# Performance work log

Hardware: AMD Instinct MI355X
Metric: run time of the kernel (lower is better)

The kernel has to match this reference:

```python
import jax, jax.numpy as jnp
import numpy as np

D_MODEL, Q, V, H = 1024, 64, 64, 16
B, K = 2, 2048


def setup_inputs() -> dict:
    key = jax.random.key(0)
    ks = jax.random.split(key, 8)
    s = 0.02
    return {
        "xi": jax.random.normal(ks[0], (B, K, D_MODEL), dtype=jnp.float32),
        # stacked per-head projection weights (equivalent to h separate nn.Linear)
        "Wq": jax.random.normal(ks[1], (H, D_MODEL, Q), dtype=jnp.float32) * s,
        "bq": jax.random.normal(ks[2], (H, Q), dtype=jnp.float32) * s,
        "Wk": jax.random.normal(ks[3], (H, D_MODEL, Q), dtype=jnp.float32) * s,
        "bk": jax.random.normal(ks[4], (H, Q), dtype=jnp.float32) * s,
        "Wv": jax.random.normal(ks[5], (H, D_MODEL, V), dtype=jnp.float32) * s,
        "bv": jax.random.normal(ks[6], (H, V), dtype=jnp.float32) * s,
        "Wo": jax.random.normal(ks[7], (H * V, D_MODEL), dtype=jnp.float32) * s,
        "bo": jnp.zeros((D_MODEL,), dtype=jnp.float32),
    }


def reference(xi, Wq, bq, Wk, bk, Wv, bv, Wo, bo):
    # per-head projections, batched over heads: [B,H,K,q]
    queries = jnp.einsum("bkd,hdq->bhkq", xi, Wq) + bq[None, :, None, :]
    keys = jnp.einsum("bkd,hdq->bhkq", xi, Wk) + bk[None, :, None, :]
    values = jnp.einsum("bkd,hdv->bhkv", xi, Wv) + bv[None, :, None, :]
    # NOTE: original scales by sqrt(queries.shape[1]) == sqrt(seq_len K), not sqrt(q)
    scale = 1.0 / np.sqrt(xi.shape[1]).astype(np.float32)
    scores = jax.nn.softmax(jnp.einsum("bhkq,bhmq->bhkm", queries, keys) * scale, axis=-1)
    attn = jnp.einsum("bhkm,bhmv->bhkv", scores, values)  # [B,H,K,v]
    # concat heads along last dim -> [B,K,H*v]
    attn = attn.transpose(0, 2, 1, 3).reshape(xi.shape[0], xi.shape[1], -1)
    return attn @ Wo + bo
```

## Files before the change

### kernel.cpp

```cpp
#include <hip/hip_runtime.h>
#include <math.h>

typedef __bf16 bf16x8 __attribute__((ext_vector_type(8)));
typedef float  f32x4  __attribute__((ext_vector_type(4)));
typedef float  f32x16 __attribute__((ext_vector_type(16)));
typedef unsigned short u16x8 __attribute__((ext_vector_type(8)));
typedef unsigned short u16x4 __attribute__((ext_vector_type(4)));

#define D_MODEL 1024
#define QDIM    64
#define HEADS   16
#define BATCH   2
#define SEQ     2048
#define M_ROWS  (BATCH*SEQ)
#define NCAT    (HEADS*3*QDIM)

__device__ __forceinline__ unsigned short f2bf(float f) {
    unsigned int u = __float_as_uint(f);
    u += 0x7fffu + ((u >> 16) & 1u);
    return (unsigned short)(u >> 16);
}

__device__ __forceinline__ void gl16(const unsigned short* g, unsigned short* l) {
    __builtin_amdgcn_global_load_lds(
        (const __attribute__((address_space(1))) unsigned int*)g,
        (__attribute__((address_space(3))) unsigned int*)l, 16, 0, 0);
}

__global__ __launch_bounds__(256) void k_cvt_bf16(const float* __restrict__ in,
                                                  unsigned short* __restrict__ out) {
    int i = (blockIdx.x * 256 + threadIdx.x) * 8;
    f32x4 a = *(const f32x4*)(in + i);
    f32x4 b = *(const f32x4*)(in + i + 4);
    u16x8 o;
    o[0]=f2bf(a[0]); o[1]=f2bf(a[1]); o[2]=f2bf(a[2]); o[3]=f2bf(a[3]);
    o[4]=f2bf(b[0]); o[5]=f2bf(b[1]); o[6]=f2bf(b[2]); o[7]=f2bf(b[3]);
    *(u16x8*)(out + i) = o;
}

__global__ __launch_bounds__(256) void k_prep_w(const float* __restrict__ Wq,
                                                const float* __restrict__ Wk,
                                                const float* __restrict__ Wv,
                                                const float* __restrict__ bq,
                                                const float* __restrict__ bk,
                                                const float* __restrict__ bv,
                                                const float* __restrict__ Wo,
                                                unsigned short* __restrict__ WcatT,
                                                float* __restrict__ bcat,
                                                unsigned short* __restrict__ WoT,
                                                float qscale) {
    __shared__ float t[64][65];
    int tid = threadIdx.x;
    int dr = tid >> 2, qc = (tid & 3) * 16;
    if (blockIdx.x < 768) {
        int blk = blockIdx.x;
        int dt = blk & 15, h = (blk >> 4) & 15, s = blk >> 8;
        const float* W = (s == 0) ? Wq : (s == 1) ? Wk : Wv;
        float sc = (s == 0) ? qscale : 1.0f;
        const float* src = W + (size_t)h * (D_MODEL * QDIM) + (size_t)(dt * 64 + dr) * QDIM + qc;
#pragma unroll
        for (int j = 0; j < 4; ++j) {
            f32x4 v = *(const f32x4*)(src + j * 4);
            t[dr][qc + j * 4 + 0] = v[0]; t[dr][qc + j * 4 + 1] = v[1];
            t[dr][qc + j * 4 + 2] = v[2]; t[dr][qc + j * 4 + 3] = v[3];
        }
        __syncthreads();
        int q = tid >> 2, dc = (tid & 3) * 16;
        unsigned short* dst = WcatT + (size_t)(h * 192 + s * 64 + q) * D_MODEL + dt * 64 + dc;
#pragma unroll
        for (int j = 0; j < 2; ++j) {
            u16x8 o;
#pragma unroll
            for (int e = 0; e < 8; ++e) o[e] = f2bf(t[dc + j * 8 + e][q] * sc);
            *(u16x8*)(dst + j * 8) = o;
        }
        if (dt == 0 && tid < 64) {
            const float* bb = (s == 0) ? bq : (s == 1) ? bk : bv;
            bcat[h * 192 + s * 64 + tid] = bb[h * QDIM + tid] * sc;
        }
    } else {
        int blk = blockIdx.x - 768;
        int ct = blk & 15, rt = blk >> 4;
        const float* src = Wo + (size_t)(rt * 64 + dr) * D_MODEL + ct * 64 + qc;
#pragma unroll
        for (int j = 0; j < 4; ++j) {
            f32x4 v = *(const f32x4*)(src + j * 4);
            t[dr][qc + j * 4 + 0] = v[0]; t[dr][qc + j * 4 + 1] = v[1];
            t[dr][qc + j * 4 + 2] = v[2]; t[dr][qc + j * 4 + 3] = v[3];
        }
        __syncthreads();
        int q = tid >> 2, dc = (tid & 3) * 16;
        unsigned short* dst = WoT + (size_t)(ct * 64 + q) * D_MODEL + rt * 64 + dc;
#pragma unroll
        for (int j = 0; j < 2; ++j) {
            u16x8 o;
#pragma unroll
            for (int e = 0; e < 8; ++e) o[e] = f2bf(t[dc + j * 8 + e][q]);
            *(u16x8*)(dst + j * 8) = o;
        }
    }
}

template<bool FUSED>
__global__ __launch_bounds__(256) void k_gemm(const unsigned short* __restrict__ A,
                                              const unsigned short* __restrict__ BT,
                                              const float* __restrict__ bias,
                                              void* __restrict__ Cout,
                                              unsigned short* __restrict__ kfrag,
                                              unsigned short* __restrict__ vfrag,
                                              int N, int Kd) {
    __shared__ __align__(16) unsigned char smem[65536];
    const int tid = threadIdx.x;
    const int lane = tid & 63, w = tid >> 6;
    const int g = lane >> 4, c = lane & 15;
    int nwg = gridDim.x * gridDim.y;
    int bid = blockIdx.y * gridDim.x + blockIdx.x;
    int sw = (bid & 7) * (nwg >> 3) + (bid >> 3);
    int bx = sw % gridDim.x, by = sw / gridDim.x;
    const int m0 = by * 128, n0 = bx * 128;
    const int wm = (w >> 1) * 64, wn = (w & 1) * 64;
    f32x4 acc[4][4] = {};

    const int srow = w * 16 + (lane >> 2);
    const int scol = ((lane & 3) ^ ((lane >> 3) & 3)) * 8;
    const unsigned short* pA0 = A  + (size_t)(m0 + srow) * Kd + scol;
    const unsigned short* pA1 = pA0 + (size_t)64 * Kd;
    const unsigned short* pB0 = BT + (size_t)(n0 + srow) * Kd + scol;
    const unsigned short* pB1 = pB0 + (size_t)64 * Kd;
    const int kc = (c >> 1) & 3;
    const int aoff = (wm + c) * 64 + ((g ^ kc) * 16);
    const int boff = (wn + c) * 64 + ((g ^ kc) * 16);

#define STAGE(buf)                                                                   \
    {                                                                                \
        unsigned short* lb = (unsigned short*)(smem + (buf) * 16384) + w * 512;      \
        gl16(pA0, lb);                                                               \
        gl16(pA1, lb + 2048);                                                        \
        gl16(pB0, lb + 4096);                                                        \
        gl16(pB1, lb + 6144);                                                        \
        pA0 += 32; pA1 += 32; pB0 += 32; pB1 += 32;                                  \
    }

#define COMPUTE(buf)                                                                 \
    {                                                                                \
        const unsigned char* Ab = smem + (buf) * 16384;                              \
        const unsigned char* Bb = Ab + 8192;                                         \
        bf16x8 af[4], bfr[4];                                                        \
        _Pragma("unroll") for (int mf = 0; mf < 4; ++mf)                             \
            af[mf] = *(const bf16x8*)(Ab + mf * 1024 + aoff);                        \
        _Pragma("unroll") for (int nf = 0; nf < 4; ++nf)                             \
            bfr[nf] = *(const bf16x8*)(Bb + nf * 1024 + boff);                       \
        __builtin_amdgcn_s_setprio(1);                                               \
        _Pragma("unroll") for (int mf = 0; mf < 4; ++mf)                             \
            _Pragma("unroll") for (int nf = 0; nf < 4; ++nf)                         \
                acc[mf][nf] = __builtin_amdgcn_mfma_f32_16x16x32_bf16(               \
                    af[mf], bfr[nf], acc[mf][nf], 0, 0, 0);                          \
        __builtin_amdgcn_s_setprio(0);                                               \
    }

    const int nt = Kd >> 5;
    STAGE(0); STAGE(1); STAGE(2);

    for (int t = 0; t < nt - 3; ++t) {
        STAGE((t + 3) & 3);
        asm volatile("s_waitcnt vmcnt(12)" ::: "memory");
        __builtin_amdgcn_s_barrier();
        __builtin_amdgcn_sched_barrier(0);
        COMPUTE(t & 3);
        __builtin_amdgcn_sched_barrier(0);
        __builtin_amdgcn_s_barrier();
    }
    asm volatile("s_waitcnt vmcnt(8)" ::: "memory");
    __builtin_amdgcn_s_barrier();
    __builtin_amdgcn_sched_barrier(0);
    COMPUTE((nt - 3) & 3);
    __builtin_amdgcn_sched_barrier(0);
    __builtin_amdgcn_s_barrier();
    asm volatile("s_waitcnt vmcnt(4)" ::: "memory");
    __builtin_amdgcn_s_barrier();
    __builtin_amdgcn_sched_barrier(0);
    COMPUTE((nt - 2) & 3);
    __builtin_amdgcn_sched_barrier(0);
    __builtin_amdgcn_s_barrier();
    asm volatile("s_waitcnt vmcnt(0)" ::: "memory");
    __builtin_amdgcn_s_barrier();
    __builtin_amdgcn_sched_barrier(0);
    COMPUTE((nt - 1) & 3);
#undef STAGE
#undef COMPUTE

#pragma unroll
    for (int mf = 0; mf < 4; ++mf) {
        const int row0 = m0 + wm + mf * 16 + 4 * g;
        const int bb_  = row0 >> 11;
        const int s_   = row0 & 2047;
        const int tile = s_ >> 6;
        const int krb  = s_ & 63;
#pragma unroll
        for (int nf = 0; nf < 4; ++nf) {
            int col = n0 + wn + nf * 16 + c;
            float bv = bias[col];
            if (!FUSED) {
#pragma unroll
                for (int r = 0; r < 4; ++r)
                    ((float*)Cout)[(size_t)(row0 + r) * N + col] = acc[mf][nf][r] + bv;
            } else {
                unsigned short q0 = f2bf(acc[mf][nf][0] + bv);
                unsigned short q1 = f2bf(acc[mf][nf][1] + bv);
                unsigned short q2 = f2bf(acc[mf][nf][2] + bv);
                unsigned short q3 = f2bf(acc[mf][nf][3] + bv);
                int h   = col / 192;
                int rem = col - h * 192;
                int kind = rem >> 6;
                int d   = rem & 63;
                if (kind == 0) {
                    unsigned short* p = (unsigned short*)Cout + (size_t)row0 * NCAT + col;
                    p[0] = q0; p[NCAT] = q1; p[2 * NCAT] = q2; p[3 * NCAT] = q3;
                } else {
                    size_t obase = (size_t)(bb_ * 512 + h * 32 + tile) * 4096;
                    if (kind == 1) {
                        int f  = (krb >> 5) * 4 + (d >> 4);
                        int hi = (d >> 3) & 1;
                        unsigned short* p = kfrag + obase + f * 512 + hi * 256 +
                                            (size_t)(krb & 31) * 8 + (d & 7);
                        p[0] = q0; p[8] = q1; p[16] = q2; p[24] = q3;
                    } else {
                        int f  = (krb >> 5) * 4 + ((krb >> 4) & 1) * 2 + (d >> 5);
                        int hi = (krb >> 3) & 1;
                        u16x4 pk = {q0, q1, q2, q3};
                        *(u16x4*)(vfrag + obase + f * 512 + hi * 256 +
                                  (size_t)(d & 31) * 8 + (krb & 7)) = pk;
                    }
                }
            }
        }
    }
}

__global__ __launch_bounds__(256) void k_attn(const unsigned short* __restrict__ qkv,
                                              const unsigned short* __restrict__ kfrag,
                                              const unsigned short* __restrict__ vfrag,
                                              unsigned short* __restrict__ attn) {
    int bid = blockIdx.x;
    int blk = (bid & 7) * 128 + (bid >> 3);
    int qt = blk & 31, h = (blk >> 5) & 15, b = blk >> 9;
    int tid = threadIdx.x, w = tid >> 6, lane = tid & 63;
    int l31 = lane & 31, hi = lane >> 5;
    int qh = w & 1, kh = w >> 1;

    __shared__ float red[4096];
    __shared__ float rsb[128];

    const int qbase = b * SEQ + qt * 64;
    const unsigned short* qrow = qkv + (size_t)(qbase + qh * 32 + l31) * NCAT + h * 192;
    bf16x8 qf0 = *(const bf16x8*)(qrow + 0 * 16 + hi * 8);
    bf16x8 qf1 = *(const bf16x8*)(qrow + 1 * 16 + hi * 8);
    bf16x8 qf2 = *(const bf16x8*)(qrow + 2 * 16 + hi * 8);
    bf16x8 qf3 = *(const bf16x8*)(qrow + 3 * 16 + hi * 8);

    f32x16 o0 = {}, o1 = {};
    float rsum = 0.f;

    const size_t fb = (size_t)(b * 512 + h * 32) * 4096 + (size_t)(kh * 4) * 512 + lane * 8;
    const unsigned short* kp = kfrag + fb;
    const unsigned short* vp = vfrag + fb;

    bf16x8 aK0, aK1, aK2, aK3, aV0, aV1, aV2, aV3;
    bf16x8 bK0, bK1, bK2, bK3, bV0, bV1, bV2, bV3;

#define LOADT(K0, K1, K2, K3, V0, V1, V2, V3)                   \
    {                                                           \
        K0 = *(const bf16x8*)(kp);                              \
        K1 = *(const bf16x8*)(kp + 512);                        \
        K2 = *(const bf16x8*)(kp + 1024);                       \
        K3 = *(const bf16x8*)(kp + 1536);                       \
        V0 = *(const bf16x8*)(vp);                              \
        V1 = *(const bf16x8*)(vp + 512);                        \
        V2 = *(const bf16x8*)(vp + 1024);                       \
        V3 = *(const bf16x8*)(vp + 1536);                       \
        kp += 4096; vp += 4096;                                 \
    }

#define COMPUTE(K0, K1, K2, K3, V0, V1, V2, V3)                                       \
    {                                                                                 \
        f32x16 st = {};                                                               \
        st = __builtin_amdgcn_mfma_f32_32x32x16_bf16(K0, qf0, st, 0, 0, 0);           \
        st = __builtin_amdgcn_mfma_f32_32x32x16_bf16(K1, qf1, st, 0, 0, 0);           \
        st = __builtin_amdgcn_mfma_f32_32x32x16_bf16(K2, qf2, st, 0, 0, 0);           \
        st = __builtin_amdgcn_mfma_f32_32x32x16_bf16(K3, qf3, st, 0, 0, 0);           \
        _Pragma("unroll") for (int r = 0; r < 16; ++r) {                              \
            float p = __builtin_amdgcn_exp2f(st[r]);                                  \
            st[r] = p;                                                                \
            rsum += p;                                                                \
        }                                                                             \
        unsigned int d0, d1, d2, d3, d4, d5, d6, d7;                                  \
        asm("v_cvt_pk_bf16_f32 %0, %1, %2" : "=v"(d0) : "v"(st[0]),  "v"(st[1]));     \
        asm("v_cvt_pk_bf16_f32 %0, %1, %2" : "=v"(d1) : "v"(st[2]),  "v"(st[3]));     \
        asm("v_cvt_pk_bf16_f32 %0, %1, %2" : "=v"(d2) : "v"(st[4]),  "v"(st[5]));     \
        asm("v_cvt_pk_bf16_f32 %0, %1, %2" : "=v"(d3) : "v"(st[6]),  "v"(st[7]));     \
        asm("v_cvt_pk_bf16_f32 %0, %1, %2" : "=v"(d4) : "v"(st[8]),  "v"(st[9]));     \
        asm("v_cvt_pk_bf16_f32 %0, %1, %2" : "=v"(d5) : "v"(st[10]), "v"(st[11]));    \
        asm("v_cvt_pk_bf16_f32 %0, %1, %2" : "=v"(d6) : "v"(st[12]), "v"(st[13]));    \
        asm("v_cvt_pk_bf16_f32 %0, %1, %2" : "=v"(d7) : "v"(st[14]), "v"(st[15]));    \
        asm("v_permlane32_swap_b32 %0, %1" : "+v"(d0), "+v"(d2));                     \
        asm("v_permlane32_swap_b32 %0, %1" : "+v"(d1), "+v"(d3));                     \
        asm("v_permlane32_swap_b32 %0, %1" : "+v"(d4), "+v"(d6));                     \
        asm("v_permlane32_swap_b32 %0, %1" : "+v"(d5), "+v"(d7));                     \
        union { unsigned int u[4]; bf16x8 v; } pa0, pa1;                              \
        pa0.u[0] = d0; pa0.u[1] = d1; pa0.u[2] = d2; pa0.u[3] = d3;                   \
        pa1.u[0] = d4; pa1.u[1] = d5; pa1.u[2] = d6; pa1.u[3] = d7;                   \
        o0 = __builtin_amdgcn_mfma_f32_32x32x16_bf16(pa0.v, V0, o0, 0, 0, 0);         \
        o1 = __builtin_amdgcn_mfma_f32_32x32x16_bf16(pa0.v, V1, o1, 0, 0, 0);         \
        o0 = __builtin_amdgcn_mfma_f32_32x32x16_bf16(pa1.v, V2, o0, 0, 0, 0);         \
        o1 = __builtin_amdgcn_mfma_f32_32x32x16_bf16(pa1.v, V3, o1, 0, 0, 0);         \
    }

    LOADT(aK0, aK1, aK2, aK3, aV0, aV1, aV2, aV3);

    const int NT = SEQ / 64;
    for (int t = 0; t < NT; t += 2) {
        LOADT(bK0, bK1, bK2, bK3, bV0, bV1, bV2, bV3);
        COMPUTE(aK0, aK1, aK2, aK3, aV0, aV1, aV2, aV3);
        if (t + 2 < NT)
            LOADT(aK0, aK1, aK2, aK3, aV0, aV1, aV2, aV3);
        COMPUTE(bK0, bK1, bK2, bK3, bV0, bV1, bV2, bV3);
    }
#undef LOADT
#undef COMPUTE

    rsum += __shfl_xor(rsum, 32);
    if (kh == 1) {
#pragma unroll
        for (int r = 0; r < 16; ++r) {
            int q = (r & 3) + 8 * (r >> 2) + 4 * hi;
            red[(qh * 32 + q) * 64 + l31]      = o0[r];
            red[(qh * 32 + q) * 64 + 32 + l31] = o1[r];
        }
    }
    if (lane < 32) rsb[(kh * 2 + qh) * 32 + l31] = rsum;
    __syncthreads();
    if (kh == 0) {
#pragma unroll
        for (int r = 0; r < 16; ++r) {
            int q = (r & 3) + 8 * (r >> 2) + 4 * hi;
            float tot = rsb[qh * 32 + q] + rsb[(2 + qh) * 32 + q];
            float inv = 1.0f / tot;
            float v0e = (o0[r] + red[(qh * 32 + q) * 64 + l31]) * inv;
            float v1e = (o1[r] + red[(qh * 32 + q) * 64 + 32 + l31]) * inv;
            int row = qbase + qh * 32 + q;
            attn[(size_t)row * (HEADS * QDIM) + h * QDIM + l31]      = f2bf(v0e);
            attn[(size_t)row * (HEADS * QDIM) + h * QDIM + 32 + l31] = f2bf(v1e);
        }
    }
}

extern "C" void kernel_launch(void* const* d_in, const int* in_sizes, int n_in,
                              void* d_out, int out_size, void* d_ws, size_t ws_size,
                              hipStream_t stream) {
    const float* xi = (const float*)d_in[0];
    const float* Wq = (const float*)d_in[1];
    const float* bq = (const float*)d_in[2];
    const float* Wk = (const float*)d_in[3];
    const float* bk = (const float*)d_in[4];
    const float* Wv = (const float*)d_in[5];
    const float* bv = (const float*)d_in[6];
    const float* Wo = (const float*)d_in[7];
    const float* bo = (const float*)d_in[8];

    unsigned short* xi_bf = (unsigned short*)d_ws;
    unsigned short* WcatT = xi_bf + (size_t)M_ROWS * D_MODEL;
    unsigned short* WoT   = WcatT + (size_t)NCAT * D_MODEL;
    float*          bcat  = (float*)(WoT + (size_t)D_MODEL * D_MODEL);
    unsigned short* qkvc  = (unsigned short*)(bcat + NCAT);
    unsigned short* kfrag = qkvc + (size_t)M_ROWS * NCAT;
    unsigned short* vfrag = kfrag + (size_t)BATCH * HEADS * 32 * 4096;
    unsigned short* attnb = vfrag + (size_t)BATCH * HEADS * 32 * 4096;

    float qscale = 1.4426950408889634f / sqrtf((float)SEQ);

    k_cvt_bf16<<<(M_ROWS * D_MODEL) / 2048, 256, 0, stream>>>(xi, xi_bf);
    k_prep_w<<<1024, 256, 0, stream>>>(Wq, Wk, Wv, bq, bk, bv, Wo, WcatT, bcat, WoT, qscale);

    k_gemm<true><<<dim3(NCAT / 128, M_ROWS / 128), 256, 0, stream>>>(
        xi_bf, WcatT, bcat, (void*)qkvc, kfrag, vfrag, NCAT, D_MODEL);

    k_attn<<<BATCH * HEADS * (SEQ / 64), 256, 0, stream>>>(qkvc, kfrag, vfrag, attnb);

    k_gemm<false><<<dim3(D_MODEL / 128, M_ROWS / 128), 256, 0, stream>>>(
        attnb, WoT, bo, d_out, nullptr, nullptr, D_MODEL, D_MODEL);
}
```

Before: 116.9 us.

## Merge input conversion into weight prep kernel and use 3-stage GEMM pipeline

The fp32-to-bf16 conversion of xi is folded into the weight-prep kernel as extra blocks, which removes one kernel launch and lets the two independent conversions overlap. The GEMM's LDS ring buffer drops from four stages to three (64KB to 48KB of shared memory), with the wait counts adjusted to match. The smaller LDS footprint may allow more workgroups per CU, at the cost of less prefetch depth for hiding global-load latency.

```diff
diff --git a/kernel.cpp b/kernel.cpp
--- a/kernel.cpp
+++ b/kernel.cpp
@@ -27,33 +27,34 @@
         (__attribute__((address_space(3))) unsigned int*)l, 16, 0, 0);
 }
 
-__global__ __launch_bounds__(256) void k_cvt_bf16(const float* __restrict__ in,
-                                                  unsigned short* __restrict__ out) {
-    int i = (blockIdx.x * 256 + threadIdx.x) * 8;
-    f32x4 a = *(const f32x4*)(in + i);
-    f32x4 b = *(const f32x4*)(in + i + 4);
-    u16x8 o;
-    o[0]=f2bf(a[0]); o[1]=f2bf(a[1]); o[2]=f2bf(a[2]); o[3]=f2bf(a[3]);
-    o[4]=f2bf(b[0]); o[5]=f2bf(b[1]); o[6]=f2bf(b[2]); o[7]=f2bf(b[3]);
-    *(u16x8*)(out + i) = o;
-}
-
-__global__ __launch_bounds__(256) void k_prep_w(const float* __restrict__ Wq,
+__global__ __launch_bounds__(256) void k_prep_w(const float* __restrict__ xi,
+                                                const float* __restrict__ Wq,
                                                 const float* __restrict__ Wk,
                                                 const float* __restrict__ Wv,
                                                 const float* __restrict__ bq,
                                                 const float* __restrict__ bk,
                                                 const float* __restrict__ bv,
                                                 const float* __restrict__ Wo,
+                                                unsigned short* __restrict__ xi_bf,
                                                 unsigned short* __restrict__ WcatT,
                                                 float* __restrict__ bcat,
                                                 unsigned short* __restrict__ WoT,
                                                 float qscale) {
+    int tid = threadIdx.x;
+    if (blockIdx.x < 2048) {
+        int i = (blockIdx.x * 256 + tid) * 8;
+        f32x4 a = *(const f32x4*)(xi + i);
+        f32x4 b = *(const f32x4*)(xi + i + 4);
+        u16x8 o;
+        o[0]=f2bf(a[0]); o[1]=f2bf(a[1]); o[2]=f2bf(a[2]); o[3]=f2bf(a[3]);
+        o[4]=f2bf(b[0]); o[5]=f2bf(b[1]); o[6]=f2bf(b[2]); o[7]=f2bf(b[3]);
+        *(u16x8*)(xi_bf + i) = o;
+        return;
+    }
     __shared__ float t[64][65];
-    int tid = threadIdx.x;
     int dr = tid >> 2, qc = (tid & 3) * 16;
-    if (blockIdx.x < 768) {
-        int blk = blockIdx.x;
+    if (blockIdx.x < 2816) {
+        int blk = blockIdx.x - 2048;
         int dt = blk & 15, h = (blk >> 4) & 15, s = blk >> 8;
         const float* W = (s == 0) ? Wq : (s == 1) ? Wk : Wv;
         float sc = (s == 0) ? qscale : 1.0f;
@@ -79,7 +80,7 @@
             bcat[h * 192 + s * 64 + tid] = bb[h * QDIM + tid] * sc;
         }
     } else {
-        int blk = blockIdx.x - 768;
+        int blk = blockIdx.x - 2816;
         int ct = blk & 15, rt = blk >> 4;
         const float* src = Wo + (size_t)(rt * 64 + dr) * D_MODEL + ct * 64 + qc;
 #pragma unroll
@@ -109,7 +110,7 @@
                                               unsigned short* __restrict__ kfrag,
                                               unsigned short* __restrict__ vfrag,
                                               int N, int Kd) {
-    __shared__ __align__(16) unsigned char smem[65536];
+    __shared__ __align__(16) unsigned char smem[49152];
     const int tid = threadIdx.x;
     const int lane = tid & 63, w = tid >> 6;
     const int g = lane >> 4, c = lane & 15;
@@ -159,33 +160,30 @@
     }
 
     const int nt = Kd >> 5;
-    STAGE(0); STAGE(1); STAGE(2);
-
-    for (int t = 0; t < nt - 3; ++t) {
-        STAGE((t + 3) & 3);
-        asm volatile("s_waitcnt vmcnt(12)" ::: "memory");
+    STAGE(0); STAGE(1);
+    int sb = 2, cb = 0;
+    for (int t = 0; t < nt - 2; ++t) {
+        STAGE(sb);
+        sb = (sb == 2) ? 0 : sb + 1;
+        asm volatile("s_waitcnt vmcnt(8)" ::: "memory");
         __builtin_amdgcn_s_barrier();
         __builtin_amdgcn_sched_barrier(0);
-        COMPUTE(t & 3);
+        COMPUTE(cb);
+        cb = (cb == 2) ? 0 : cb + 1;
         __builtin_amdgcn_sched_barrier(0);
         __builtin_amdgcn_s_barrier();
     }
-    asm volatile("s_waitcnt vmcnt(8)" ::: "memory");
-    __builtin_amdgcn_s_barrier();
-    __builtin_amdgcn_sched_barrier(0);
-    COMPUTE((nt - 3) & 3);
-    __builtin_amdgcn_sched_barrier(0);
-    __builtin_amdgcn_s_barrier();
     asm volatile("s_waitcnt vmcnt(4)" ::: "memory");
     __builtin_amdgcn_s_barrier();
     __builtin_amdgcn_sched_barrier(0);
-    COMPUTE((nt - 2) & 3);
+    COMPUTE(cb);
+    cb = (cb == 2) ? 0 : cb + 1;
     __builtin_amdgcn_sched_barrier(0);
     __builtin_amdgcn_s_barrier();
     asm volatile("s_waitcnt vmcnt(0)" ::: "memory");
     __builtin_amdgcn_s_barrier();
     __builtin_amdgcn_sched_barrier(0);
-    COMPUTE((nt - 1) & 3);
+    COMPUTE(cb);
 #undef STAGE
 #undef COMPUTE
 
@@ -378,8 +376,8 @@
 
     float qscale = 1.4426950408889634f / sqrtf((float)SEQ);
 
-    k_cvt_bf16<<<(M_ROWS * D_MODEL) / 2048, 256, 0, stream>>>(xi, xi_bf);
-    k_prep_w<<<1024, 256, 0, stream>>>(Wq, Wk, Wv, bq, bk, bv, Wo, WcatT, bcat, WoT, qscale);
+    k_prep_w<<<3072, 256, 0, stream>>>(xi, Wq, Wk, Wv, bq, bk, bv, Wo,
+                                       xi_bf, WcatT, bcat, WoT, qscale);
 
     k_gemm<true><<<dim3(NCAT / 128, M_ROWS / 128), 256, 0, stream>>>(
         xi_bf, WcatT, bcat, (void*)qkvc, kfrag, vfrag, NCAT, D_MODEL);
```

Result: faster. 114.4 us (median of 3 runs) (-2.2%).
